# Kernel tuning notes

Measured on AMD Instinct MI355X. Metric: run time of the kernel, lower is better.

Reference implementation:

```python
import jax, jax.numpy as jnp
import numpy as np

F, H, B, T_IN, T_OUT, D_OUT, L = 8, 512, 256, 336, 96, 2, 2
G = 4 * H  # gate dim (i, f, g, o per PyTorch order)
SCALE = 0.04  # ~1/sqrt(H), matches torch LSTM init magnitude


def setup_inputs() -> dict:
    key = jax.random.key(0)
    ks = jax.random.split(key, 18)
    r = lambda k, shp: (jax.random.normal(k, shp, dtype=jnp.float32) * SCALE)
    inp = {
        "src": jax.random.normal(ks[0], (B, T_IN, F), dtype=jnp.float32),
        "enc_Wih0": r(ks[1], (G, F)),
        "enc_Whh0": r(ks[2], (G, H)),
        "enc_b0": r(ks[3], (G,)),
        "enc_Wih1": r(ks[4], (G, H)),
        "enc_Whh1": r(ks[5], (G, H)),
        "enc_b1": r(ks[6], (G,)),
        "dec_Wih0": r(ks[7], (G, F)),
        "dec_Whh0": r(ks[8], (G, H)),
        "dec_b0": r(ks[9], (G,)),
        "dec_Wih1": r(ks[10], (G, H)),
        "dec_Whh1": r(ks[11], (G, H)),
        "dec_b1": r(ks[12], (G,)),
        "fc_W": r(ks[13], (D_OUT, H)),
        "fc_b": r(ks[14], (D_OUT,)),
        "proj_W": r(ks[15], (F, D_OUT)),
        "proj_b": r(ks[16], (F,)),
    }
    return inp


def lstm_cell(x, h, c, Wih, Whh, b):
    # x: [B, in], h/c: [B, H]; PyTorch gate order i, f, g, o
    gates = x @ Wih.T + h @ Whh.T + b
    i, f, g, o = jnp.split(gates, 4, axis=-1)
    c_new = jax.nn.sigmoid(f) * c + jax.nn.sigmoid(i) * jnp.tanh(g)
    h_new = jax.nn.sigmoid(o) * jnp.tanh(c_new)
    return h_new, c_new


def run_lstm_layer(xs, Wih, Whh, b):
    # xs: [T, B, in] -> outputs [T, B, H], final (h, c)
    bsz = xs.shape[1]
    h0 = jnp.zeros((bsz, Whh.shape[1]), xs.dtype)

    def step(carry, x):
        h, c = carry
        h, c = lstm_cell(x, h, c, Wih, Whh, b)
        return (h, c), h

    (h, c), ys = jax.lax.scan(step, (h0, h0), xs)
    return ys, h, c


def reference(src, enc_Wih0, enc_Whh0, enc_b0, enc_Wih1, enc_Whh1, enc_b1,
              dec_Wih0, dec_Whh0, dec_b0, dec_Wih1, dec_Whh1, dec_b1,
              fc_W, fc_b, proj_W, proj_b):
    # ----- encoder (2-layer LSTM over the input window) -----
    xs = jnp.transpose(src, (1, 0, 2))  # [T_IN, B, F]
    ys0, h0, c0 = run_lstm_layer(xs, enc_Wih0, enc_Whh0, enc_b0)
    _, h1, c1 = run_lstm_layer(ys0, enc_Wih1, enc_Whh1, enc_b1)

    pred0 = src[:, -1, :][:, jnp.array([0, 2])]  # [B, 2]

    def dec_step(carry, _):
        h0, c0, h1, c1, pred = carry
        x = pred @ proj_W.T + proj_b                      # proj: output_dim -> num_features
        h0, c0 = lstm_cell(x, h0, c0, dec_Wih0, dec_Whh0, dec_b0)
        h1, c1 = lstm_cell(h0, h1, c1, dec_Wih1, dec_Whh1, dec_b1)
        pred = h1 @ fc_W.T + fc_b                         # fc: hidden -> output_dim
        return (h0, c0, h1, c1, pred), pred

    _, preds = jax.lax.scan(dec_step, (h0, c0, h1, c1, pred0), None, length=T_OUT)
    return jnp.transpose(preds, (1, 0, 2))  # [B, T_OUT, 2]
```

## Files before the change

### kernel.cpp

```cpp
#include <hip/hip_runtime.h>
#include <hip/hip_fp16.h>
#include <math.h>

#define F 8
#define T_IN 336
#define T_OUT 96
#define D_OUT 2
#define NGRP 16
#define WPG 32
#define ROWS 16
#define NT 512
#define HROW 2048

#define WE0 0
#define WE1 1048576
#define WD0 3145728
#define WD1 4194304
#define W_TOTAL 6291456
#define HO0 0
#define HO1 262144
#define HBUF 131072

using f32x4 = __attribute__((ext_vector_type(4))) float;
using f16x8 = __attribute__((ext_vector_type(8))) _Float16;

struct Args {
  const float *src;
  const float *eWih0, *eb0, *eb1;
  const float *dWih0, *db0, *db1;
  const float *fcW, *fcb, *pW, *pb;
  const unsigned short *W;
  unsigned short *Hst;
  float *out;
  unsigned *cnt;
};

__device__ __forceinline__ float sigm(float x) { return 1.f / (1.f + __expf(-x)); }
__device__ __forceinline__ float tanh_f(float x) {
  float e = __expf(-2.f * fabsf(x));
  float r = (1.f - e) / (1.f + e);
  return copysignf(r, x);
}
__device__ __forceinline__ f32x4 mfma16(f16x8 a, f16x8 b, f32x4 c) {
  return __builtin_amdgcn_mfma_f32_16x16x32_f16(a, b, c, 0, 0, 0);
}
__device__ __forceinline__ void ld16_cg(uint4& d, const void* p) {
  asm volatile("global_load_dwordx4 %0, %1, off sc0 sc1" : "=v"(d) : "v"(p));
}
__device__ __forceinline__ void st2_cg(void* p, unsigned v) {
  asm volatile("global_store_short %0, %1, off sc0 sc1" :: "v"(p), "v"(v) : "memory");
}

__global__ __launch_bounds__(256) void conv_kernel(
    const float* eWhh0, const float* eWih1, const float* eWhh1,
    const float* dWhh0, const float* dWih1, const float* dWhh1,
    unsigned short* W) {
  size_t i = (size_t)blockIdx.x * 256 + threadIdx.x;
  if (i >= W_TOTAL) return;
  int set, j;
  if (i < WE1)      { set = 0; j = (int)i; }
  else if (i < WD0) { set = 1; j = (int)(i - WE1); }
  else if (i < WD1) { set = 2; j = (int)(i - WD0); }
  else              { set = 3; j = (int)(i - WD1); }
  const int big = (set == 1 || set == 3);
  const int e = j & 7, lane = (j >> 3) & 63, r = j >> 9;
  const int kb = big ? (r & 31) : (r & 15);
  const int sw = big ? (r >> 5) : (r >> 4);
  const int s = sw >> 2, w = sw & 3;
  const int c = lane & 15;
  const int n = (c & 3) * 512 + 16 * s + 4 * w + (c >> 2);
  const int k = kb * 32 + (lane >> 4) * 8 + e;
  float v;
  if (set == 0)      v = eWhh0[(size_t)n * 512 + k];
  else if (set == 1) v = (k < 512) ? eWih1[(size_t)n * 512 + k] : eWhh1[(size_t)n * 512 + k - 512];
  else if (set == 2) v = dWhh0[(size_t)n * 512 + k];
  else               v = (k < 512) ? dWih1[(size_t)n * 512 + k] : dWhh1[(size_t)n * 512 + k - 512];
  W[i] = __half_as_ushort(__float2half_rn(v));
}

__global__ __launch_bounds__(NT, 2) void forecast_kernel(Args a) {
  extern __shared__ char smem[];
  char* HCa = smem;
  char* HCb = smem + 32768;
  float* TT = (float*)(smem + 65536);
  float* p_lds = TT + 8 * 288;
  float* x_lds = p_lds + 32;
  float* WxL = x_lds + 144;
  float* bL = WxL + 1152;
  float* pWb = bL + 256;

  const int tid = threadIdx.x;
  const int pr = blockIdx.x >> 5;
  const int s = blockIdx.x & 31;
  const int gA = pr * 2, gB = pr * 2 + 1;
  const int lane = tid & 63, wid = tid >> 6;
  const int bb = lane & 15;
  const int lq = lane >> 4;
  const int isL0 = (wid < 4);
  const int w4 = isL0 ? wid : wid - 4;
  const int uu = lane >> 4;
  const int unitL = w4 * 4 + uu;
  float* TTw = TT + wid * 288;
  unsigned* slotA = a.cnt + gA * 32;
  unsigned* slotB = a.cnt + gB * 32;
  unsigned bsA = 0, bsB = 0;

  const int nkbE = isL0 ? 16 : 32;
  const unsigned short* wE = a.W + (isL0 ? WE0 : WE1) + (size_t)(s * 4 + w4) * nkbE * 512 + lane * 8;
  const unsigned short* wD = a.W + (isL0 ? WD0 : WD1) + (size_t)(s * 4 + w4) * nkbE * 512 + lane * 8;

  f16x8 wreg[32];
  auto loadW = [&](const unsigned short* wp) {
    #pragma unroll
    for (int kb = 0; kb < 32; ++kb)
      if (kb < nkbE) wreg[kb] = *(const f16x8*)(wp + (size_t)kb * 512);
  };
  loadW(wE);

  for (int e = tid; e < 1152; e += NT) {
    int set = e / 576, e2 = e % 576, row = e2 / 9, k = e2 % 9;
    const float* sw = set ? a.dWih0 : a.eWih0;
    WxL[e] = (k < 8) ? sw[(size_t)((row >> 4) * 512 + 16 * s + (row & 15)) * 8 + k] : 0.f;
  }
  if (tid < 256) {
    int bs = tid >> 6, q = (tid >> 4) & 3, u2 = tid & 15;
    const float* sp = bs == 0 ? a.eb0 : bs == 1 ? a.eb1 : bs == 2 ? a.db0 : a.db1;
    bL[tid] = sp[q * 512 + 16 * s + u2];
  }
  if (tid < 16) pWb[tid] = a.pW[tid];
  else if (tid < 24) pWb[tid] = a.pb[tid - 16];
  else if (tid < 26) pWb[tid] = a.fcb[tid - 24];
  __syncthreads();

  float cA = 0.f, cB = 0.f;
  const int srow = tid >> 5, seg = tid & 31;
  const int wswz = (srow & 7) << 4;
  const int aswz = (bb & 7) << 4;

  auto waitG = [&](unsigned* slots, unsigned target) {
    if (wid == 0) {
      long gd = 0;
      for (;;) {
        unsigned v = (lane < 32 && lane != s)
            ? __hip_atomic_load(slots + lane, __ATOMIC_RELAXED, __HIP_MEMORY_SCOPE_AGENT)
            : target;
        if (__all((int)(v >= target))) break;
        __builtin_amdgcn_s_sleep(1);
        if (++gd > (1L << 16)) break;
      }
    }
    __syncthreads();
    asm volatile("" ::: "memory");
  };
  auto arriveG = [&](unsigned* slots, unsigned target) {
    asm volatile("s_waitcnt vmcnt(0)" ::: "memory");
    __syncthreads();
    if (tid == 0)
      __hip_atomic_store(slots + s, target, __ATOMIC_RELAXED, __HIP_MEMORY_SCOPE_AGENT);
  };

  auto stage2 = [&](char* HC, const unsigned short* b0, const unsigned short* b1, int g) {
    const unsigned short* p0 = b0 + (size_t)(16 * g + srow) * 512 + seg * 8;
    const unsigned short* p1 = b1 + (size_t)(16 * g + srow) * 512 + seg * 8;
    uint4 q0, q1, q2, q3;
    ld16_cg(q0, p0); ld16_cg(q1, p0 + 256); ld16_cg(q2, p1); ld16_cg(q3, p1 + 256);
    asm volatile("s_waitcnt vmcnt(0)" ::: "memory");
    __builtin_amdgcn_sched_barrier(0);
    char* d = HC + srow * HROW + ((seg * 16) ^ wswz);
    *(uint4*)d = q0; *(uint4*)(d + 512) = q1;
    *(uint4*)(d + 1024) = q2; *(uint4*)(d + 1536) = q3;
  };
  auto stage1 = [&](char* HC, const unsigned short* b0, int plane, int g) {
    const unsigned short* p0 = b0 + (size_t)(16 * g + srow) * 512 + seg * 8;
    uint4 q0, q1;
    ld16_cg(q0, p0); ld16_cg(q1, p0 + 256);
    asm volatile("s_waitcnt vmcnt(0)" ::: "memory");
    __builtin_amdgcn_sched_barrier(0);
    char* d = HC + srow * HROW + plane + ((seg * 16) ^ wswz);
    *(uint4*)d = q0; *(uint4*)(d + 512) = q1;
  };
  auto fcw = [&](char* HC, int g, int t) {
    const int pb_ = lane & 15, dd = (lane >> 4) & 1, hf = lane >> 5;
    const char* hp = HC + pb_ * HROW;
    const int fswz = (pb_ & 7) << 4;
    const float* wr = a.fcW + dd * 512 + hf * 256;
    float r = 0.f;
    #pragma unroll 8
    for (int j = 0; j < 32; ++j) {
      f16x8 v = *(const f16x8*)(hp + ((1024 + hf * 512 + j * 16) ^ fswz));
      float4 w0 = *(const float4*)(wr + j * 8);
      float4 w1 = *(const float4*)(wr + j * 8 + 4);
      r = fmaf((float)v[0], w0.x, r); r = fmaf((float)v[1], w0.y, r);
      r = fmaf((float)v[2], w0.z, r); r = fmaf((float)v[3], w0.w, r);
      r = fmaf((float)v[4], w1.x, r); r = fmaf((float)v[5], w1.y, r);
      r = fmaf((float)v[6], w1.z, r); r = fmaf((float)v[7], w1.w, r);
    }
    r += __shfl_xor(r, 32);
    if (lane < 32) {
      float pred = r + pWb[24 + dd];
      if (t == 0) pred = a.src[(size_t)(16 * g + pb_) * (T_IN * F) + 335 * F + dd * 2];
      p_lds[pb_ * 2 + dd] = pred;
      if (s == 0 && t > 0)
        a.out[(size_t)(16 * g + pb_) * (T_OUT * D_OUT) + (size_t)(t - 1) * D_OUT + dd] = pred;
    }
    const int bx = lane >> 2, j0 = (lane & 3) * 2;
    float pr0 = p_lds[bx * 2], pr1 = p_lds[bx * 2 + 1];
    x_lds[bx * 9 + j0]     = pWb[16 + j0]     + pr0 * pWb[j0 * 2]       + pr1 * pWb[j0 * 2 + 1];
    x_lds[bx * 9 + j0 + 1] = pWb[16 + j0 + 1] + pr0 * pWb[(j0 + 1) * 2] + pr1 * pWb[(j0 + 1) * 2 + 1];
  };

  auto encPhase = [&](char* HC, unsigned* slots, unsigned& bs, float& c01, int g, int t) {
    waitG(slots, bs);
    const int buf = t & 1, nbuf = buf ^ 1;
    stage2(HC, a.Hst + HO0 + (size_t)buf * HBUF, a.Hst + HO1 + (size_t)buf * HBUF, g);
    __syncthreads();
    const bool active = isL0 ? (t < T_IN) : (t >= 1);
    if (active) {
      f32x4 acc = {0.f, 0.f, 0.f, 0.f};
      const char* arow = HC + bb * HROW;
      #pragma unroll
      for (int kb = 0; kb < 32; ++kb)
        if (kb < nkbE)
          acc = mfma16(*(const f16x8*)(arow + ((lq * 16 + kb * 64) ^ aswz)), wreg[kb], acc);
      #pragma unroll
      for (int j = 0; j < 4; ++j) TTw[bb * 18 + lq * 4 + j] = acc[j];
      float ac[4];
      #pragma unroll
      for (int q = 0; q < 4; ++q)
        ac[q] = TTw[(4 * uu + q) * 18 + bb] + bL[(isL0 ? 0 : 64) + q * 16 + unitL];
      const int rowG = 16 * g + bb;
      if (isL0) {
        const float* xr = a.src + (size_t)rowG * (T_IN * F) + t * F;
        float4 x0 = *(const float4*)xr, x1 = *(const float4*)(xr + 4);
        float xv[8] = {x0.x, x0.y, x0.z, x0.w, x1.x, x1.y, x1.z, x1.w};
        #pragma unroll
        for (int q = 0; q < 4; ++q)
          #pragma unroll
          for (int k = 0; k < 8; ++k)
            ac[q] = fmaf(xv[k], WxL[(q * 16 + unitL) * 9 + k], ac[q]);
      }
      c01 = sigm(ac[1]) * c01 + sigm(ac[0]) * tanh_f(ac[2]);
      float h = sigm(ac[3]) * tanh_f(c01);
      unsigned short* hplane = a.Hst + (isL0 ? HO0 : HO1) + (size_t)nbuf * HBUF;
      st2_cg((void*)(hplane + (size_t)rowG * 512 + 16 * s + unitL),
             (unsigned)__half_as_ushort(__float2half_rn(h)));
    }
    arriveG(slots, ++bs);
  };

  auto decP1 = [&](char* HC, unsigned* slots, unsigned& bs, float& c01, int g, int t) {
    waitG(slots, bs);
    const int pA = t & 1;
    stage1(HC, a.Hst + HO1 + (size_t)(pA ^ 1) * HBUF, 1024, g);
    __syncthreads();
    if (isL0) {
      f32x4 acc = {0.f, 0.f, 0.f, 0.f};
      const char* arow = HC + bb * HROW;
      #pragma unroll
      for (int kb = 0; kb < 16; ++kb)
        acc = mfma16(*(const f16x8*)(arow + ((lq * 16 + kb * 64) ^ aswz)), wreg[kb], acc);
      #pragma unroll
      for (int j = 0; j < 4; ++j) TTw[bb * 18 + lq * 4 + j] = acc[j];
    } else if (wid == 4) {
      fcw(HC, g, t);
    }
    __syncthreads();
    if (isL0) {
      float ac[4];
      #pragma unroll
      for (int q = 0; q < 4; ++q)
        ac[q] = TTw[(4 * uu + q) * 18 + bb] + bL[128 + q * 16 + unitL];
      #pragma unroll
      for (int q = 0; q < 4; ++q)
        #pragma unroll
        for (int k = 0; k < 8; ++k)
          ac[q] = fmaf(x_lds[bb * 9 + k], WxL[576 + (q * 16 + unitL) * 9 + k], ac[q]);
      c01 = sigm(ac[1]) * c01 + sigm(ac[0]) * tanh_f(ac[2]);
      float h = sigm(ac[3]) * tanh_f(c01);
      unsigned short* hplane = a.Hst + HO0 + (size_t)(pA ^ 1) * HBUF;
      st2_cg((void*)(hplane + (size_t)(16 * g + bb) * 512 + 16 * s + unitL),
             (unsigned)__half_as_ushort(__float2half_rn(h)));
    }
    arriveG(slots, ++bs);
  };

  auto decP2 = [&](char* HC, unsigned* slots, unsigned& bs, float& c01, int g, int t) {
    waitG(slots, bs);
    const int pA = t & 1;
    stage1(HC, a.Hst + HO0 + (size_t)(pA ^ 1) * HBUF, 0, g);
    __syncthreads();
    if (!isL0) {
      f32x4 acc = {0.f, 0.f, 0.f, 0.f};
      const char* arow = HC + bb * HROW;
      #pragma unroll
      for (int kb = 0; kb < 32; ++kb)
        acc = mfma16(*(const f16x8*)(arow + ((lq * 16 + kb * 64) ^ aswz)), wreg[kb], acc);
      #pragma unroll
      for (int j = 0; j < 4; ++j) TTw[bb * 18 + lq * 4 + j] = acc[j];
      float ac[4];
      #pragma unroll
      for (int q = 0; q < 4; ++q)
        ac[q] = TTw[(4 * uu + q) * 18 + bb] + bL[192 + q * 16 + unitL];
      c01 = sigm(ac[1]) * c01 + sigm(ac[0]) * tanh_f(ac[2]);
      float h = sigm(ac[3]) * tanh_f(c01);
      unsigned short* hplane = a.Hst + HO1 + (size_t)pA * HBUF;
      st2_cg((void*)(hplane + (size_t)(16 * g + bb) * 512 + 16 * s + unitL),
             (unsigned)__half_as_ushort(__float2half_rn(h)));
    }
    arriveG(slots, ++bs);
  };

  auto epi = [&](char* HC, unsigned* slots, unsigned& bs, int g) {
    waitG(slots, bs);
    stage1(HC, a.Hst + HO1 + (size_t)1 * HBUF, 1024, g);
    __syncthreads();
    if (wid == 4 && s == 0) {
      const int pb_ = lane & 15, dd = (lane >> 4) & 1, hf = lane >> 5;
      const char* hp = HC + pb_ * HROW;
      const int fswz = (pb_ & 7) << 4;
      const float* wr = a.fcW + dd * 512 + hf * 256;
      float r = 0.f;
      #pragma unroll 8
      for (int j = 0; j < 32; ++j) {
        f16x8 v = *(const f16x8*)(hp + ((1024 + hf * 512 + j * 16) ^ fswz));
        float4 w0 = *(const float4*)(wr + j * 8);
        float4 w1 = *(const float4*)(wr + j * 8 + 4);
        r = fmaf((float)v[0], w0.x, r); r = fmaf((float)v[1], w0.y, r);
        r = fmaf((float)v[2], w0.z, r); r = fmaf((float)v[3], w0.w, r);
        r = fmaf((float)v[4], w1.x, r); r = fmaf((float)v[5], w1.y, r);
        r = fmaf((float)v[6], w1.z, r); r = fmaf((float)v[7], w1.w, r);
      }
      r += __shfl_xor(r, 32);
      if (lane < 32)
        a.out[(size_t)(16 * g + pb_) * (T_OUT * D_OUT) + (size_t)95 * D_OUT + dd] = r + pWb[24 + dd];
    }
    __syncthreads();
  };

  for (int t = 0; t <= T_IN; ++t) {
    encPhase(HCa, slotA, bsA, cA, gA, t);
    encPhase(HCb, slotB, bsB, cB, gB, t);
  }
  loadW(wD);
  for (int t = 0; t < T_OUT; ++t) {
    decP1(HCa, slotA, bsA, cA, gA, t);
    decP1(HCb, slotB, bsB, cB, gB, t);
    decP2(HCa, slotA, bsA, cA, gA, t);
    decP2(HCb, slotB, bsB, cB, gB, t);
  }
  epi(HCa, slotA, bsA, gA);
  epi(HCb, slotB, bsB, gB);
}

extern "C" void kernel_launch(void* const* d_in, const int* in_sizes, int n_in,
                              void* d_out, int out_size, void* d_ws, size_t ws_size,
                              hipStream_t stream) {
  (void)in_sizes; (void)n_in; (void)out_size; (void)ws_size;
  const float* src   = (const float*)d_in[0];
  const float* eWih0 = (const float*)d_in[1];
  const float* eWhh0 = (const float*)d_in[2];
  const float* eb0   = (const float*)d_in[3];
  const float* eWih1 = (const float*)d_in[4];
  const float* eWhh1 = (const float*)d_in[5];
  const float* eb1   = (const float*)d_in[6];
  const float* dWih0 = (const float*)d_in[7];
  const float* dWhh0 = (const float*)d_in[8];
  const float* db0   = (const float*)d_in[9];
  const float* dWih1 = (const float*)d_in[10];
  const float* dWhh1 = (const float*)d_in[11];
  const float* db1   = (const float*)d_in[12];
  const float* fcW   = (const float*)d_in[13];
  const float* fcb   = (const float*)d_in[14];
  const float* pW    = (const float*)d_in[15];
  const float* pb    = (const float*)d_in[16];

  unsigned char* ws = (unsigned char*)d_ws;
  unsigned* cnt = (unsigned*)ws;
  unsigned short* W = (unsigned short*)(ws + 4096);
  unsigned short* Hst = W + W_TOTAL;

  (void)hipMemsetAsync(d_ws, 0, 4096, stream);
  (void)hipMemsetAsync((void*)Hst, 0, (size_t)4 * HBUF * sizeof(unsigned short), stream);

  hipLaunchKernelGGL(conv_kernel, dim3(W_TOTAL / 256), dim3(256), 0, stream,
                     eWhh0, eWih1, eWhh1, dWhh0, dWih1, dWhh1, W);

  Args a;
  a.src = src; a.eWih0 = eWih0; a.eb0 = eb0; a.eb1 = eb1;
  a.dWih0 = dWih0; a.db0 = db0; a.db1 = db1;
  a.fcW = fcW; a.fcb = fcb; a.pW = pW; a.pb = pb;
  a.W = W; a.Hst = Hst; a.out = (float*)d_out; a.cnt = cnt;

  const size_t smem_bytes = 65536 + (2304 + 32 + 144 + 1152 + 256 + 32) * sizeof(float);
  hipLaunchKernelGGL(forecast_kernel, dim3((NGRP / 2) * WPG), dim3(NT), smem_bytes, stream, a);
}
```

Baseline: 3.416 ms.

## Software-pipeline hidden-state loads across the two batch groups to overlap barrier waits

Splits each phase into issue/write/compute pieces and interleaves the two batch groups. The global loads of the next group's hidden state are issued before the current group's h stores have drained, with partial vmcnt waits, so load latency overlaps with publishing. Arrival is signalled after a partial wait that only covers the stores. This adds ordering subtlety in the cross-block sync protocol and could race or deadlock if the counts are wrong.

```diff
diff --git a/kernel.cpp b/kernel.cpp
--- a/kernel.cpp
+++ b/kernel.cpp
@@ -50,6 +50,9 @@
 __device__ __forceinline__ void st2_cg(void* p, unsigned v) {
   asm volatile("global_store_short %0, %1, off sc0 sc1" :: "v"(p), "v"(v) : "memory");
 }
+__device__ __forceinline__ void vw0() { asm volatile("s_waitcnt vmcnt(0)" ::: "memory"); }
+__device__ __forceinline__ void vw2() { asm volatile("s_waitcnt vmcnt(2)" ::: "memory"); }
+__device__ __forceinline__ void vw4() { asm volatile("s_waitcnt vmcnt(4)" ::: "memory"); }
 
 __global__ __launch_bounds__(256) void conv_kernel(
     const float* eWhh0, const float* eWih1, const float* eWhh1,
@@ -105,6 +108,9 @@
   unsigned* slotB = a.cnt + gB * 32;
   unsigned bsA = 0, bsB = 0;
 
+  unsigned short* H0 = a.Hst + HO0;
+  unsigned short* H1 = a.Hst + HO1;
+
   const int nkbE = isL0 ? 16 : 32;
   const unsigned short* wE = a.W + (isL0 ? WE0 : WE1) + (size_t)(s * 4 + w4) * nkbE * 512 + lane * 8;
   const unsigned short* wD = a.W + (isL0 ? WD0 : WD1) + (size_t)(s * 4 + w4) * nkbE * 512 + lane * 8;
@@ -137,7 +143,9 @@
   const int wswz = (srow & 7) << 4;
   const int aswz = (bb & 7) << 4;
 
-  auto waitG = [&](unsigned* slots, unsigned target) {
+  uint4 pf0, pf1, pf2, pf3;
+
+  auto pollG = [&](unsigned* slots, unsigned target) {
     if (wid == 0) {
       long gd = 0;
       for (;;) {
@@ -152,33 +160,70 @@
     __syncthreads();
     asm volatile("" ::: "memory");
   };
-  auto arriveG = [&](unsigned* slots, unsigned target) {
-    asm volatile("s_waitcnt vmcnt(0)" ::: "memory");
-    __syncthreads();
+  auto pub = [&](unsigned* slots, unsigned target) {
     if (tid == 0)
       __hip_atomic_store(slots + s, target, __ATOMIC_RELAXED, __HIP_MEMORY_SCOPE_AGENT);
   };
-
-  auto stage2 = [&](char* HC, const unsigned short* b0, const unsigned short* b1, int g) {
+  auto issue2 = [&](const unsigned short* b0, const unsigned short* b1, int g) {
     const unsigned short* p0 = b0 + (size_t)(16 * g + srow) * 512 + seg * 8;
     const unsigned short* p1 = b1 + (size_t)(16 * g + srow) * 512 + seg * 8;
-    uint4 q0, q1, q2, q3;
-    ld16_cg(q0, p0); ld16_cg(q1, p0 + 256); ld16_cg(q2, p1); ld16_cg(q3, p1 + 256);
-    asm volatile("s_waitcnt vmcnt(0)" ::: "memory");
+    ld16_cg(pf0, p0); ld16_cg(pf1, p0 + 256); ld16_cg(pf2, p1); ld16_cg(pf3, p1 + 256);
+  };
+  auto issue1 = [&](const unsigned short* b0, int g) {
+    const unsigned short* p0 = b0 + (size_t)(16 * g + srow) * 512 + seg * 8;
+    ld16_cg(pf0, p0); ld16_cg(pf1, p0 + 256);
+  };
+  auto write2 = [&](char* HC) {
+    vw0();
     __builtin_amdgcn_sched_barrier(0);
     char* d = HC + srow * HROW + ((seg * 16) ^ wswz);
-    *(uint4*)d = q0; *(uint4*)(d + 512) = q1;
-    *(uint4*)(d + 1024) = q2; *(uint4*)(d + 1536) = q3;
-  };
-  auto stage1 = [&](char* HC, const unsigned short* b0, int plane, int g) {
-    const unsigned short* p0 = b0 + (size_t)(16 * g + srow) * 512 + seg * 8;
-    uint4 q0, q1;
-    ld16_cg(q0, p0); ld16_cg(q1, p0 + 256);
-    asm volatile("s_waitcnt vmcnt(0)" ::: "memory");
+    *(uint4*)d = pf0; *(uint4*)(d + 512) = pf1;
+    *(uint4*)(d + 1024) = pf2; *(uint4*)(d + 1536) = pf3;
+    __syncthreads();
+  };
+  auto write1 = [&](char* HC, int plane) {
+    vw0();
     __builtin_amdgcn_sched_barrier(0);
     char* d = HC + srow * HROW + plane + ((seg * 16) ^ wswz);
-    *(uint4*)d = q0; *(uint4*)(d + 512) = q1;
-  };
+    *(uint4*)d = pf0; *(uint4*)(d + 512) = pf1;
+    __syncthreads();
+  };
+
+  auto encCompute = [&](char* HC, float& c01, int g, int t) {
+    const int nbuf = (t & 1) ^ 1;
+    const bool active = isL0 ? (t < T_IN) : (t >= 1);
+    if (active) {
+      f32x4 acc = {0.f, 0.f, 0.f, 0.f};
+      const char* arow = HC + bb * HROW;
+      #pragma unroll
+      for (int kb = 0; kb < 32; ++kb)
+        if (kb < nkbE)
+          acc = mfma16(*(const f16x8*)(arow + ((lq * 16 + kb * 64) ^ aswz)), wreg[kb], acc);
+      #pragma unroll
+      for (int j = 0; j < 4; ++j) TTw[bb * 18 + lq * 4 + j] = acc[j];
+      float ac[4];
+      #pragma unroll
+      for (int q = 0; q < 4; ++q)
+        ac[q] = TTw[(4 * uu + q) * 18 + bb] + bL[(isL0 ? 0 : 64) + q * 16 + unitL];
+      const int rowG = 16 * g + bb;
+      if (isL0) {
+        const float* xr = a.src + (size_t)rowG * (T_IN * F) + t * F;
+        float4 x0 = *(const float4*)xr, x1 = *(const float4*)(xr + 4);
+        float xv[8] = {x0.x, x0.y, x0.z, x0.w, x1.x, x1.y, x1.z, x1.w};
+        #pragma unroll
+        for (int q = 0; q < 4; ++q)
+          #pragma unroll
+          for (int k = 0; k < 8; ++k)
+            ac[q] = fmaf(xv[k], WxL[(q * 16 + unitL) * 9 + k], ac[q]);
+      }
+      c01 = sigm(ac[1]) * c01 + sigm(ac[0]) * tanh_f(ac[2]);
+      float h = sigm(ac[3]) * tanh_f(c01);
+      unsigned short* hplane = (isL0 ? H0 : H1) + (size_t)nbuf * HBUF;
+      st2_cg((void*)(hplane + (size_t)rowG * 512 + 16 * s + unitL),
+             (unsigned)__half_as_ushort(__float2half_rn(h)));
+    }
+  };
+
   auto fcw = [&](char* HC, int g, int t) {
     const int pb_ = lane & 15, dd = (lane >> 4) & 1, hf = lane >> 5;
     const char* hp = HC + pb_ * HROW;
@@ -209,50 +254,8 @@
     x_lds[bx * 9 + j0 + 1] = pWb[16 + j0 + 1] + pr0 * pWb[(j0 + 1) * 2] + pr1 * pWb[(j0 + 1) * 2 + 1];
   };
 
-  auto encPhase = [&](char* HC, unsigned* slots, unsigned& bs, float& c01, int g, int t) {
-    waitG(slots, bs);
-    const int buf = t & 1, nbuf = buf ^ 1;
-    stage2(HC, a.Hst + HO0 + (size_t)buf * HBUF, a.Hst + HO1 + (size_t)buf * HBUF, g);
-    __syncthreads();
-    const bool active = isL0 ? (t < T_IN) : (t >= 1);
-    if (active) {
-      f32x4 acc = {0.f, 0.f, 0.f, 0.f};
-      const char* arow = HC + bb * HROW;
-      #pragma unroll
-      for (int kb = 0; kb < 32; ++kb)
-        if (kb < nkbE)
-          acc = mfma16(*(const f16x8*)(arow + ((lq * 16 + kb * 64) ^ aswz)), wreg[kb], acc);
-      #pragma unroll
-      for (int j = 0; j < 4; ++j) TTw[bb * 18 + lq * 4 + j] = acc[j];
-      float ac[4];
-      #pragma unroll
-      for (int q = 0; q < 4; ++q)
-        ac[q] = TTw[(4 * uu + q) * 18 + bb] + bL[(isL0 ? 0 : 64) + q * 16 + unitL];
-      const int rowG = 16 * g + bb;
-      if (isL0) {
-        const float* xr = a.src + (size_t)rowG * (T_IN * F) + t * F;
-        float4 x0 = *(const float4*)xr, x1 = *(const float4*)(xr + 4);
-        float xv[8] = {x0.x, x0.y, x0.z, x0.w, x1.x, x1.y, x1.z, x1.w};
-        #pragma unroll
-        for (int q = 0; q < 4; ++q)
-          #pragma unroll
-          for (int k = 0; k < 8; ++k)
-            ac[q] = fmaf(xv[k], WxL[(q * 16 + unitL) * 9 + k], ac[q]);
-      }
-      c01 = sigm(ac[1]) * c01 + sigm(ac[0]) * tanh_f(ac[2]);
-      float h = sigm(ac[3]) * tanh_f(c01);
-      unsigned short* hplane = a.Hst + (isL0 ? HO0 : HO1) + (size_t)nbuf * HBUF;
-      st2_cg((void*)(hplane + (size_t)rowG * 512 + 16 * s + unitL),
-             (unsigned)__half_as_ushort(__float2half_rn(h)));
-    }
-    arriveG(slots, ++bs);
-  };
-
-  auto decP1 = [&](char* HC, unsigned* slots, unsigned& bs, float& c01, int g, int t) {
-    waitG(slots, bs);
+  auto decCompute1 = [&](char* HC, float& c01, int g, int t) {
     const int pA = t & 1;
-    stage1(HC, a.Hst + HO1 + (size_t)(pA ^ 1) * HBUF, 1024, g);
-    __syncthreads();
     if (isL0) {
       f32x4 acc = {0.f, 0.f, 0.f, 0.f};
       const char* arow = HC + bb * HROW;
@@ -277,18 +280,14 @@
           ac[q] = fmaf(x_lds[bb * 9 + k], WxL[576 + (q * 16 + unitL) * 9 + k], ac[q]);
       c01 = sigm(ac[1]) * c01 + sigm(ac[0]) * tanh_f(ac[2]);
       float h = sigm(ac[3]) * tanh_f(c01);
-      unsigned short* hplane = a.Hst + HO0 + (size_t)(pA ^ 1) * HBUF;
+      unsigned short* hplane = H0 + (size_t)(pA ^ 1) * HBUF;
       st2_cg((void*)(hplane + (size_t)(16 * g + bb) * 512 + 16 * s + unitL),
              (unsigned)__half_as_ushort(__float2half_rn(h)));
     }
-    arriveG(slots, ++bs);
-  };
-
-  auto decP2 = [&](char* HC, unsigned* slots, unsigned& bs, float& c01, int g, int t) {
-    waitG(slots, bs);
+  };
+
+  auto decCompute2 = [&](char* HC, float& c01, int g, int t) {
     const int pA = t & 1;
-    stage1(HC, a.Hst + HO0 + (size_t)(pA ^ 1) * HBUF, 0, g);
-    __syncthreads();
     if (!isL0) {
       f32x4 acc = {0.f, 0.f, 0.f, 0.f};
       const char* arow = HC + bb * HROW;
@@ -303,17 +302,13 @@
         ac[q] = TTw[(4 * uu + q) * 18 + bb] + bL[192 + q * 16 + unitL];
       c01 = sigm(ac[1]) * c01 + sigm(ac[0]) * tanh_f(ac[2]);
       float h = sigm(ac[3]) * tanh_f(c01);
-      unsigned short* hplane = a.Hst + HO1 + (size_t)pA * HBUF;
+      unsigned short* hplane = H1 + (size_t)pA * HBUF;
       st2_cg((void*)(hplane + (size_t)(16 * g + bb) * 512 + 16 * s + unitL),
              (unsigned)__half_as_ushort(__float2half_rn(h)));
     }
-    arriveG(slots, ++bs);
-  };
-
-  auto epi = [&](char* HC, unsigned* slots, unsigned& bs, int g) {
-    waitG(slots, bs);
-    stage1(HC, a.Hst + HO1 + (size_t)1 * HBUF, 1024, g);
-    __syncthreads();
+  };
+
+  auto epiCompute = [&](char* HC, int g) {
     if (wid == 4 && s == 0) {
       const int pb_ = lane & 15, dd = (lane >> 4) & 1, hf = lane >> 5;
       const char* hp = HC + pb_ * HROW;
@@ -334,22 +329,64 @@
       if (lane < 32)
         a.out[(size_t)(16 * g + pb_) * (T_OUT * D_OUT) + (size_t)95 * D_OUT + dd] = r + pWb[24 + dd];
     }
-    __syncthreads();
-  };
+  };
+
+  pollG(slotA, bsA);
+  issue2(H0 + 0 * HBUF, H1 + 0 * HBUF, gA);
 
   for (int t = 0; t <= T_IN; ++t) {
-    encPhase(HCa, slotA, bsA, cA, gA, t);
-    encPhase(HCb, slotB, bsB, cB, gB, t);
+    const size_t bo = (size_t)(t & 1) * HBUF;
+    write2(HCa);
+    encCompute(HCa, cA, gA, t);
+    pollG(slotB, bsB);
+    issue2(H0 + bo, H1 + bo, gB);
+    vw4(); __syncthreads(); pub(slotA, ++bsA);
+    write2(HCb);
+    encCompute(HCb, cB, gB, t);
+    pollG(slotA, bsA);
+    if (t < T_IN) {
+      const size_t bn = (size_t)((t + 1) & 1) * HBUF;
+      issue2(H0 + bn, H1 + bn, gA);
+      vw4();
+    } else {
+      issue1(H1 + 1 * HBUF, gA);
+      vw2();
+    }
+    __syncthreads(); pub(slotB, ++bsB);
   }
+
   loadW(wD);
+
   for (int t = 0; t < T_OUT; ++t) {
-    decP1(HCa, slotA, bsA, cA, gA, t);
-    decP1(HCb, slotB, bsB, cB, gB, t);
-    decP2(HCa, slotA, bsA, cA, gA, t);
-    decP2(HCb, slotB, bsB, cB, gB, t);
+    const int pA = t & 1;
+    write1(HCa, 1024);
+    decCompute1(HCa, cA, gA, t);
+    pollG(slotB, bsB);
+    issue1(H1 + (size_t)(pA ^ 1) * HBUF, gB);
+    vw2(); __syncthreads(); pub(slotA, ++bsA);
+    write1(HCb, 1024);
+    decCompute1(HCb, cB, gB, t);
+    pollG(slotA, bsA);
+    issue1(H0 + (size_t)(pA ^ 1) * HBUF, gA);
+    vw2(); __syncthreads(); pub(slotB, ++bsB);
+    write1(HCa, 0);
+    decCompute2(HCa, cA, gA, t);
+    pollG(slotB, bsB);
+    issue1(H0 + (size_t)(pA ^ 1) * HBUF, gB);
+    vw2(); __syncthreads(); pub(slotA, ++bsA);
+    write1(HCb, 0);
+    decCompute2(HCb, cB, gB, t);
+    pollG(slotA, bsA);
+    issue1(H1 + (size_t)(((t + 1) & 1) ^ 1) * HBUF, gA);
+    vw2(); __syncthreads(); pub(slotB, ++bsB);
   }
-  epi(HCa, slotA, bsA, gA);
-  epi(HCb, slotB, bsB, gB);
+
+  write1(HCa, 1024);
+  epiCompute(HCa, gA);
+  pollG(slotB, bsB);
+  issue1(H1 + 1 * HBUF, gB);
+  write1(HCb, 1024);
+  epiCompute(HCb, gB);
 }
 
 extern "C" void kernel_launch(void* const* d_in, const int* in_sizes, int n_in,
```

New measurement: 3.143 ms. -8.0%, faster.
